# Kernel tuning notes

Measured on AMD Instinct MI355X. Metric: run time of the kernel, lower is better.

Reference implementation:

```python
import jax, jax.numpy as jnp
import numpy as np

N = 100000   # nodes
E = 1600000  # edges (avg degree 16), self-loops added in reference
H = 64       # hidden


def setup_inputs() -> dict:
    key = jax.random.key(0)
    k1, k2, k3, k4, k5 = jax.random.split(key, 5)
    x = jax.random.normal(k1, (N, H), dtype=jnp.float32)
    src = jax.random.randint(k2, (E,), 0, N, dtype=jnp.int32)
    off = jax.random.randint(k3, (E,), 1, N, dtype=jnp.int32)
    dst = (src + off) % N  # guaranteed no self-loops -> matches add_remaining_self_loops
    edge_index = jnp.stack([src, dst])  # row0 = j (source), row1 = i (target)
    # a_i, a_j: Linear(hidden, 1, bias=False) -> weight vectors of shape [H]
    w_i = jax.random.normal(k4, (H,), dtype=jnp.float32) / np.sqrt(H)
    w_j = jax.random.normal(k5, (H,), dtype=jnp.float32) / np.sqrt(H)
    return {"x": x, "edge_index": edge_index, "w_i": w_i, "w_j": w_j}


def reference(x, edge_index, w_i, w_j):
    n = x.shape[0]
    # add_remaining_self_loops: append (v, v) for every node (inputs have none)
    loops = jnp.arange(n, dtype=edge_index.dtype)
    src = jnp.concatenate([edge_index[0], loops])  # j
    dst = jnp.concatenate([edge_index[1], loops])  # i
    # per-node attention scalars, then per-edge gather
    s_i = x @ w_i  # [N]
    s_j = x @ w_j  # [N]
    e = jax.nn.leaky_relu(s_i[dst] + s_j[src], 0.01)  # [E+N]
    # segment softmax over destination node i (every segment non-empty via self-loop)
    e_max = jax.ops.segment_max(e, dst, num_segments=n)
    e_exp = jnp.exp(e - e_max[dst])
    denom = jax.ops.segment_sum(e_exp, dst, num_segments=n)
    alpha = e_exp / denom[dst]  # [E+N]
    # spmm: out[i] = sum_j alpha_ij * x[j], then ReLU
    out = jax.ops.segment_sum(alpha[:, None] * x[src], dst, num_segments=n)
    return jax.nn.relu(out)
```

## Files before the change

kernel.cpp:

```cpp
#include <hip/hip_runtime.h>

#define H 64
#define H4 16
#define H8 8
#define NBUCK 391
#define CAP 4608
#define BIN_BLOCKS 196
#define NODE_PER_BLK 16

typedef _Float16 half8 __attribute__((ext_vector_type(8)));


__global__ __launch_bounds__(1024) void gat_nodebin_kernel(
        const float* __restrict__ x,
        const float* __restrict__ w_i, const float* __restrict__ w_j,
        float* __restrict__ s_i, float* __restrict__ s_j,
        _Float16* __restrict__ xh,
        const int4* __restrict__ src4, const int4* __restrict__ dst4,
        int* __restrict__ cursor, int* __restrict__ buckets,
        int e4, int n) {
    __shared__ int hist[NBUCK];
    __shared__ int boff[NBUCK];
    __shared__ int boff0[NBUCK];
    __shared__ int gbase[NBUCK];
    __shared__ int wtot[16];
    __shared__ int stage[8192];

    int tid = threadIdx.x;
    int lane = tid & 63, wv = tid >> 6;

    if (blockIdx.x >= BIN_BLOCKS) {
        int node = (blockIdx.x - BIN_BLOCKS) * NODE_PER_BLK + wv;
        if (node >= n) return;
        float v = x[(long long)node * H + lane];
        xh[(long long)node * H + lane] = (_Float16)v;
        float a = v * w_i[lane];
        float b = v * w_j[lane];
        #pragma unroll
        for (int off = 32; off > 0; off >>= 1) {
            a += __shfl_down(a, off, 64);
            b += __shfl_down(b, off, 64);
        }
        if (lane == 0) { s_i[node] = a; s_j[node] = b; }
        return;
    }

    if (tid < NBUCK) hist[tid] = 0;
    __syncthreads();

    int4 s[2], d[2];
    bool val[2];
    #pragma unroll
    for (int r = 0; r < 2; ++r) {
        int i4 = blockIdx.x * 2048 + r * 1024 + tid;
        val[r] = (i4 < e4);
        if (val[r]) { s[r] = src4[i4]; d[r] = dst4[i4]; }
        else        { s[r] = make_int4(0,0,0,0); d[r] = make_int4(0,0,0,0); }
    }
    #pragma unroll
    for (int r = 0; r < 2; ++r) if (val[r]) {
        atomicAdd(&hist[d[r].x >> 8], 1);
        atomicAdd(&hist[d[r].y >> 8], 1);
        atomicAdd(&hist[d[r].z >> 8], 1);
        atomicAdd(&hist[d[r].w >> 8], 1);
    }
    __syncthreads();

    if (tid < NBUCK) gbase[tid] = atomicAdd(&cursor[tid], hist[tid]);

    int v = (tid < NBUCK) ? hist[tid] : 0;
    int incl = v;
    #pragma unroll
    for (int off = 1; off < 64; off <<= 1) {
        int t = __shfl_up(incl, off, 64);
        if (lane >= off) incl += t;
    }
    if (lane == 63) wtot[wv] = incl;
    __syncthreads();
    if (tid < NBUCK) {
        int wpref = 0;
        #pragma unroll
        for (int j = 0; j < 16; ++j) wpref += (j < wv) ? wtot[j] : 0;
        int excl = wpref + incl - v;
        boff[tid]  = excl;
        boff0[tid] = excl;
    }
    __syncthreads();

    #pragma unroll
    for (int r = 0; r < 2; ++r) if (val[r]) {
        int ss[4] = {s[r].x, s[r].y, s[r].z, s[r].w};
        int dd[4] = {d[r].x, d[r].y, d[r].z, d[r].w};
        #pragma unroll
        for (int c = 0; c < 4; ++c) {
            int b = dd[c] >> 8;
            int pos = atomicAdd(&boff[b], 1);
            stage[pos] = ((dd[c] & 255) << 17) | ss[c];
        }
    }
    __syncthreads();

    for (int b = wv; b < NBUCK; b += 16) {
        int sbase = boff0[b];
        int L = boff[b] - sbase;
        int gb = gbase[b];
        int* dstp = buckets + (long long)b * CAP + gb;
        for (int i = lane; i < L; i += 64)
            dstp[i] = stage[sbase + i];
    }
}

__global__ __launch_bounds__(1024) void gat_sort_kernel(
        const int* __restrict__ cursor, int* __restrict__ buckets,
        int* __restrict__ row_start, int* __restrict__ count, int n) {
    __shared__ int hist[256];
    __shared__ int offs[256];
    __shared__ int stage[CAP];
    __shared__ int stage2[CAP];
    __shared__ int wtot[4];

    int b = blockIdx.x;
    int tid = threadIdx.x;
    int cnt = cursor[b];
    int* bk = buckets + (long long)b * CAP;

    if (tid < 256) hist[tid] = 0;
    __syncthreads();

    for (int i = tid; i < cnt; i += 1024) {
        int w = bk[i];
        stage[i] = w;
        atomicAdd(&hist[(w >> 17) & 255], 1);
    }
    __syncthreads();

    int lane = tid & 63, wv = tid >> 6;
    int v = (tid < 256) ? hist[tid] : 0;
    int incl = v;
    #pragma unroll
    for (int off = 1; off < 64; off <<= 1) {
        int t = __shfl_up(incl, off, 64);
        if (lane >= off) incl += t;
    }
    if (tid < 256 && lane == 63) wtot[wv] = incl;
    __syncthreads();
    if (tid < 256) {
        int wpref = 0;
        #pragma unroll
        for (int j = 0; j < 4; ++j) wpref += (j < wv) ? wtot[j] : 0;
        int excl = wpref + incl - v;
        offs[tid] = excl;
        int node = (b << 8) + tid;
        if (node < n) {
            row_start[node] = b * CAP + excl;
            count[node] = v;
        }
    }
    __syncthreads();

    for (int i = tid; i < cnt; i += 1024) {
        int w = stage[i];
        int pos = atomicAdd(&offs[(w >> 17) & 255], 1);
        stage2[pos] = w & 0x1FFFF;
    }
    __syncthreads();

    for (int i = tid; i < cnt; i += 1024)
        bk[i] = stage2[i];
}

__global__ __launch_bounds__(256) void gat_aggregate_kernel(
        const float4* __restrict__ x4,
        const half8* __restrict__ xh8,
        const float* __restrict__ s_i,
        const float* __restrict__ s_j,
        const int* __restrict__ row_start,
        const int* __restrict__ count,
        const int* __restrict__ csr_src,
        float4* __restrict__ out4, int n) {
    int wid = (blockIdx.x * blockDim.x + threadIdx.x) >> 6;
    int lane = threadIdx.x & 63;
    int sub = lane >> 4;
    int l16 = lane & 15;
    int g2 = l16 >> 3;
    int q = lane & 7;

    int node = wid * 4 + sub;
    bool vnode = (node < n);
    int nsafe = vnode ? node : 0;
    float sii = s_i[nsafe];
    int start = vnode ? row_start[nsafe] : 0;
    int cnt = vnode ? count[nsafe] : 0;

    float acc[8];
    #pragma unroll
    for (int i = 0; i < 8; ++i) acc[i] = 0.f;
    float den = 0.f;

    for (int base = 0; base < cnt; base += 16) {
        int rem = cnt - base;
        int prsrc = nsafe;
        float wl = 0.f;
        if (l16 < rem) {
            prsrc = csr_src[start + base + l16];
            float e = sii + s_j[prsrc];
            e = (e >= 0.f) ? e : 0.01f * e;
            wl = __expf(e);
        }
        int sb[8]; float wb[8]; half8 hv[8];
        #pragma unroll
        for (int j = 0; j < 8; ++j) {
            int k = (sub << 4) + g2 + 2 * j;
            sb[j] = __shfl(prsrc, k, 64);
            wb[j] = __shfl(wl, k, 64);
        }
        #pragma unroll
        for (int j = 0; j < 8; ++j)
            hv[j] = xh8[(long long)sb[j] * H8 + q];
        #pragma unroll
        for (int j = 0; j < 8; ++j) {
            #pragma unroll
            for (int i = 0; i < 8; ++i)
                acc[i] = fmaf(wb[j], (float)hv[j][i], acc[i]);
            den += wb[j];
        }
    }

    #pragma unroll
    for (int i = 0; i < 8; ++i) acc[i] += __shfl_xor(acc[i], 8, 64);
    den += __shfl_xor(den, 8, 64);

    if (vnode && g2 == 0) {
        float sjn = s_j[node];
        float e0 = sii + sjn; e0 = (e0 >= 0.f) ? e0 : 0.01f * e0;
        float w0 = __expf(e0);
        float4 xa = x4[(long long)node * H4 + 2 * q];
        float4 xb = x4[(long long)node * H4 + 2 * q + 1];
        float dinv = 1.f / (den + w0);
        float4 oa, ob;
        oa.x = (acc[0] + w0 * xa.x) * dinv;
        oa.y = (acc[1] + w0 * xa.y) * dinv;
        oa.z = (acc[2] + w0 * xa.z) * dinv;
        oa.w = (acc[3] + w0 * xa.w) * dinv;
        ob.x = (acc[4] + w0 * xb.x) * dinv;
        ob.y = (acc[5] + w0 * xb.y) * dinv;
        ob.z = (acc[6] + w0 * xb.z) * dinv;
        ob.w = (acc[7] + w0 * xb.w) * dinv;
        oa.x = (oa.x > 0.f) ? oa.x : 0.f;
        oa.y = (oa.y > 0.f) ? oa.y : 0.f;
        oa.z = (oa.z > 0.f) ? oa.z : 0.f;
        oa.w = (oa.w > 0.f) ? oa.w : 0.f;
        ob.x = (ob.x > 0.f) ? ob.x : 0.f;
        ob.y = (ob.y > 0.f) ? ob.y : 0.f;
        ob.z = (ob.z > 0.f) ? ob.z : 0.f;
        ob.w = (ob.w > 0.f) ? ob.w : 0.f;
        out4[(long long)node * H4 + 2 * q]     = oa;
        out4[(long long)node * H4 + 2 * q + 1] = ob;
    }
}

extern "C" void kernel_launch(void* const* d_in, const int* in_sizes, int n_in,
                              void* d_out, int out_size, void* d_ws, size_t ws_size,
                              hipStream_t stream) {
    const float* x    = (const float*)d_in[0];
    const int*   edge = (const int*)  d_in[1];
    const float* w_i  = (const float*)d_in[2];
    const float* w_j  = (const float*)d_in[3];

    int n     = in_sizes[0] / H;
    int e_cnt = in_sizes[1] / 2;
    const int* src = edge;
    const int* dst = edge + e_cnt;

    float* out = (float*)d_out;

    char* ws = (char*)d_ws;
    float*    s_i       = (float*)ws;     ws += (size_t)n * 4;
    float*    s_j       = (float*)ws;     ws += (size_t)n * 4;
    int*      cursor    = (int*)ws;       ws += 512 * 4;
    int*      row_start = (int*)ws;       ws += (size_t)n * 4;
    int*      count     = (int*)ws;       ws += (size_t)n * 4;
    int*      buckets   = (int*)ws;       ws += (size_t)NBUCK * CAP * 4;
    _Float16* xh        = (_Float16*)ws;

    int e4 = e_cnt / 4;
    int node_blocks = (n + NODE_PER_BLK - 1) / NODE_PER_BLK;
    int fused_blocks = BIN_BLOCKS + node_blocks;

    hipMemsetAsync(cursor, 0, 512 * 4, stream);

    gat_nodebin_kernel<<<fused_blocks, 1024, 0, stream>>>(
        x, w_i, w_j, s_i, s_j, xh,
        (const int4*)src, (const int4*)dst, cursor, buckets, e4, n);

    gat_sort_kernel<<<NBUCK, 1024, 0, stream>>>(
        cursor, buckets, row_start, count, n);

    int waves = (n + 3) / 4;
    long long agg_threads = (long long)waves * 64;
    gat_aggregate_kernel<<<(unsigned)((agg_threads + 255) / 256), 256, 0, stream>>>(
        (const float4*)x, (const half8*)xh, s_i, s_j, row_start, count, buckets,
        (float4*)out, n);
}
```

Baseline: 151.6 us.

## Fuse per-bucket sort with aggregation, keeping sorted edges and weights in LDS

The separate sort kernel and aggregate kernel are merged into one kernel with one block per bucket of 256 destination nodes. The block counting-sorts the bucket's edges into shared memory and precomputes each edge's exp weight there, then aggregates its nodes directly from LDS. This removes a kernel launch, the global write and re-read of the sorted CSR, and the row_start/count arrays. In exchange, only 391 blocks of 512 threads are launched, so each block walks 256 nodes in sequence, and occupancy may be limited by the 36KB of LDS per block.

```diff
diff --git a/kernel.cpp b/kernel.cpp
--- a/kernel.cpp
+++ b/kernel.cpp
@@ -110,152 +110,164 @@
     }
 }
 
-__global__ __launch_bounds__(1024) void gat_sort_kernel(
-        const int* __restrict__ cursor, int* __restrict__ buckets,
-        int* __restrict__ row_start, int* __restrict__ count, int n) {
-    __shared__ int hist[256];
-    __shared__ int offs[256];
-    __shared__ int stage[CAP];
-    __shared__ int stage2[CAP];
-    __shared__ int wtot[4];
-
-    int b = blockIdx.x;
-    int tid = threadIdx.x;
-    int cnt = cursor[b];
-    int* bk = buckets + (long long)b * CAP;
-
-    if (tid < 256) hist[tid] = 0;
-    __syncthreads();
-
-    for (int i = tid; i < cnt; i += 1024) {
-        int w = bk[i];
-        stage[i] = w;
-        atomicAdd(&hist[(w >> 17) & 255], 1);
-    }
-    __syncthreads();
-
-    int lane = tid & 63, wv = tid >> 6;
-    int v = (tid < 256) ? hist[tid] : 0;
-    int incl = v;
-    #pragma unroll
-    for (int off = 1; off < 64; off <<= 1) {
-        int t = __shfl_up(incl, off, 64);
-        if (lane >= off) incl += t;
-    }
-    if (tid < 256 && lane == 63) wtot[wv] = incl;
-    __syncthreads();
-    if (tid < 256) {
-        int wpref = 0;
-        #pragma unroll
-        for (int j = 0; j < 4; ++j) wpref += (j < wv) ? wtot[j] : 0;
-        int excl = wpref + incl - v;
-        offs[tid] = excl;
-        int node = (b << 8) + tid;
-        if (node < n) {
-            row_start[node] = b * CAP + excl;
-            count[node] = v;
-        }
-    }
-    __syncthreads();
-
-    for (int i = tid; i < cnt; i += 1024) {
-        int w = stage[i];
-        int pos = atomicAdd(&offs[(w >> 17) & 255], 1);
-        stage2[pos] = w & 0x1FFFF;
-    }
-    __syncthreads();
-
-    for (int i = tid; i < cnt; i += 1024)
-        bk[i] = stage2[i];
-}
-
-__global__ __launch_bounds__(256) void gat_aggregate_kernel(
+__global__ __launch_bounds__(512, 4) void gat_sortagg_kernel(
         const float4* __restrict__ x4,
         const half8* __restrict__ xh8,
         const float* __restrict__ s_i,
         const float* __restrict__ s_j,
-        const int* __restrict__ row_start,
-        const int* __restrict__ count,
-        const int* __restrict__ csr_src,
+        const int* __restrict__ cursor,
+        const int* __restrict__ buckets,
         float4* __restrict__ out4, int n) {
-    int wid = (blockIdx.x * blockDim.x + threadIdx.x) >> 6;
-    int lane = threadIdx.x & 63;
+    __shared__ int   hist[256];
+    __shared__ int   offs[256];
+    __shared__ int   start0[256];
+    __shared__ float sii[256];
+    __shared__ int   wtot[8];
+    __shared__ int2  ew[CAP];
+
+    int b = blockIdx.x;
+    int tid = threadIdx.x;
+    int lane = tid & 63, wv = tid >> 6;
+    int cnt_b = cursor[b];
+    if (cnt_b > CAP) cnt_b = CAP;
+    const int* bk = buckets + (long long)b * CAP;
+
+    if (tid < 256) {
+        hist[tid] = 0;
+        int node = (b << 8) + tid;
+        sii[tid] = (node < n) ? s_i[node] : 0.f;
+    }
+    __syncthreads();
+
+    for (int i = tid; i < cnt_b; i += 512)
+        atomicAdd(&hist[(bk[i] >> 17) & 255], 1);
+    __syncthreads();
+
+    int v = (tid < 256) ? hist[tid] : 0;
+    int incl = v;
+    #pragma unroll
+    for (int off = 1; off < 64; off <<= 1) {
+        int t = __shfl_up(incl, off, 64);
+        if (lane >= off) incl += t;
+    }
+    if (tid < 256 && lane == 63) wtot[wv] = incl;
+    __syncthreads();
+    if (tid < 256) {
+        int wpref = 0;
+        #pragma unroll
+        for (int j = 0; j < 4; ++j) wpref += (j < wv) ? wtot[j] : 0;
+        int excl = wpref + incl - v;
+        offs[tid]   = excl;
+        start0[tid] = excl;
+    }
+    __syncthreads();
+
+    for (int i = tid; i < cnt_b; i += 512) {
+        int w = bk[i];
+        int loc = (w >> 17) & 255;
+        int src = w & 0x1FFFF;
+        float e = sii[loc] + s_j[src];
+        e = (e >= 0.f) ? e : 0.01f * e;
+        float we = __expf(e);
+        int pos = atomicAdd(&offs[loc], 1);
+        ew[pos] = make_int2(src, __float_as_int(we));
+    }
+    __syncthreads();
+
     int sub = lane >> 4;
-    int l16 = lane & 15;
-    int g2 = l16 >> 3;
-    int q = lane & 7;
-
-    int node = wid * 4 + sub;
-    bool vnode = (node < n);
-    int nsafe = vnode ? node : 0;
-    float sii = s_i[nsafe];
-    int start = vnode ? row_start[nsafe] : 0;
-    int cnt = vnode ? count[nsafe] : 0;
-
-    float acc[8];
-    #pragma unroll
-    for (int i = 0; i < 8; ++i) acc[i] = 0.f;
-    float den = 0.f;
-
-    for (int base = 0; base < cnt; base += 16) {
-        int rem = cnt - base;
-        int prsrc = nsafe;
-        float wl = 0.f;
-        if (l16 < rem) {
-            prsrc = csr_src[start + base + l16];
-            float e = sii + s_j[prsrc];
-            e = (e >= 0.f) ? e : 0.01f * e;
-            wl = __expf(e);
+    int g2  = (lane >> 3) & 1;
+    int q   = lane & 7;
+
+    for (int rr = 0; rr < 8; ++rr) {
+        int loc  = rr * 32 + wv * 4 + sub;
+        int node = (b << 8) + loc;
+        bool vnode = (node < n);
+        int ls   = start0[loc];
+        int cntn = vnode ? hist[loc] : 0;
+
+        float acc[8];
+        #pragma unroll
+        for (int i = 0; i < 8; ++i) acc[i] = 0.f;
+        float den = 0.f;
+
+        for (int base = 0; base < cntn; base += 16) {
+            int rem = cntn - base;
+            int lsb = ls + base + g2;
+            if (rem >= 16) {
+                int sb[8]; float wb[8]; half8 hv[8];
+                #pragma unroll
+                for (int j = 0; j < 8; ++j) {
+                    int2 e = ew[lsb + 2 * j];
+                    sb[j] = e.x; wb[j] = __int_as_float(e.y);
+                }
+                #pragma unroll
+                for (int j = 0; j < 8; ++j)
+                    hv[j] = xh8[(long long)sb[j] * H8 + q];
+                #pragma unroll
+                for (int j = 0; j < 8; ++j) {
+                    #pragma unroll
+                    for (int i = 0; i < 8; ++i)
+                        acc[i] = fmaf(wb[j], (float)hv[j][i], acc[i]);
+                    den += wb[j];
+                }
+            } else {
+                int sb[8]; float wb[8]; half8 hv[8];
+                #pragma unroll
+                for (int j = 0; j < 8; ++j) {
+                    int slot = g2 + 2 * j;
+                    sb[j] = -1; wb[j] = 0.f;
+                    if (slot < rem) {
+                        int2 e = ew[lsb + 2 * j];
+                        sb[j] = e.x; wb[j] = __int_as_float(e.y);
+                    }
+                }
+                #pragma unroll
+                for (int j = 0; j < 8; ++j)
+                    if (sb[j] >= 0)
+                        hv[j] = xh8[(long long)sb[j] * H8 + q];
+                #pragma unroll
+                for (int j = 0; j < 8; ++j) {
+                    if (sb[j] >= 0) {
+                        #pragma unroll
+                        for (int i = 0; i < 8; ++i)
+                            acc[i] = fmaf(wb[j], (float)hv[j][i], acc[i]);
+                        den += wb[j];
+                    }
+                }
+            }
         }
-        int sb[8]; float wb[8]; half8 hv[8];
-        #pragma unroll
-        for (int j = 0; j < 8; ++j) {
-            int k = (sub << 4) + g2 + 2 * j;
-            sb[j] = __shfl(prsrc, k, 64);
-            wb[j] = __shfl(wl, k, 64);
+
+        #pragma unroll
+        for (int i = 0; i < 8; ++i) acc[i] += __shfl_xor(acc[i], 8, 64);
+        den += __shfl_xor(den, 8, 64);
+
+        if (vnode && g2 == 0) {
+            float sjn = s_j[node];
+            float e0 = sii[loc] + sjn; e0 = (e0 >= 0.f) ? e0 : 0.01f * e0;
+            float w0 = __expf(e0);
+            float4 xa = x4[(long long)node * H4 + 2 * q];
+            float4 xb = x4[(long long)node * H4 + 2 * q + 1];
+            float dinv = 1.f / (den + w0);
+            float4 oa, ob;
+            oa.x = (acc[0] + w0 * xa.x) * dinv;
+            oa.y = (acc[1] + w0 * xa.y) * dinv;
+            oa.z = (acc[2] + w0 * xa.z) * dinv;
+            oa.w = (acc[3] + w0 * xa.w) * dinv;
+            ob.x = (acc[4] + w0 * xb.x) * dinv;
+            ob.y = (acc[5] + w0 * xb.y) * dinv;
+            ob.z = (acc[6] + w0 * xb.z) * dinv;
+            ob.w = (acc[7] + w0 * xb.w) * dinv;
+            oa.x = (oa.x > 0.f) ? oa.x : 0.f;
+            oa.y = (oa.y > 0.f) ? oa.y : 0.f;
+            oa.z = (oa.z > 0.f) ? oa.z : 0.f;
+            oa.w = (oa.w > 0.f) ? oa.w : 0.f;
+            ob.x = (ob.x > 0.f) ? ob.x : 0.f;
+            ob.y = (ob.y > 0.f) ? ob.y : 0.f;
+            ob.z = (ob.z > 0.f) ? ob.z : 0.f;
+            ob.w = (ob.w > 0.f) ? ob.w : 0.f;
+            out4[(long long)node * H4 + 2 * q]     = oa;
+            out4[(long long)node * H4 + 2 * q + 1] = ob;
         }
-        #pragma unroll
-        for (int j = 0; j < 8; ++j)
-            hv[j] = xh8[(long long)sb[j] * H8 + q];
-        #pragma unroll
-        for (int j = 0; j < 8; ++j) {
-            #pragma unroll
-            for (int i = 0; i < 8; ++i)
-                acc[i] = fmaf(wb[j], (float)hv[j][i], acc[i]);
-            den += wb[j];
-        }
-    }
-
-    #pragma unroll
-    for (int i = 0; i < 8; ++i) acc[i] += __shfl_xor(acc[i], 8, 64);
-    den += __shfl_xor(den, 8, 64);
-
-    if (vnode && g2 == 0) {
-        float sjn = s_j[node];
-        float e0 = sii + sjn; e0 = (e0 >= 0.f) ? e0 : 0.01f * e0;
-        float w0 = __expf(e0);
-        float4 xa = x4[(long long)node * H4 + 2 * q];
-        float4 xb = x4[(long long)node * H4 + 2 * q + 1];
-        float dinv = 1.f / (den + w0);
-        float4 oa, ob;
-        oa.x = (acc[0] + w0 * xa.x) * dinv;
-        oa.y = (acc[1] + w0 * xa.y) * dinv;
-        oa.z = (acc[2] + w0 * xa.z) * dinv;
-        oa.w = (acc[3] + w0 * xa.w) * dinv;
-        ob.x = (acc[4] + w0 * xb.x) * dinv;
-        ob.y = (acc[5] + w0 * xb.y) * dinv;
-        ob.z = (acc[6] + w0 * xb.z) * dinv;
-        ob.w = (acc[7] + w0 * xb.w) * dinv;
-        oa.x = (oa.x > 0.f) ? oa.x : 0.f;
-        oa.y = (oa.y > 0.f) ? oa.y : 0.f;
-        oa.z = (oa.z > 0.f) ? oa.z : 0.f;
-        oa.w = (oa.w > 0.f) ? oa.w : 0.f;
-        ob.x = (ob.x > 0.f) ? ob.x : 0.f;
-        ob.y = (ob.y > 0.f) ? ob.y : 0.f;
-        ob.z = (ob.z > 0.f) ? ob.z : 0.f;
-        ob.w = (ob.w > 0.f) ? ob.w : 0.f;
-        out4[(long long)node * H4 + 2 * q]     = oa;
-        out4[(long long)node * H4 + 2 * q + 1] = ob;
     }
 }
 
@@ -278,8 +290,6 @@
     float*    s_i       = (float*)ws;     ws += (size_t)n * 4;
     float*    s_j       = (float*)ws;     ws += (size_t)n * 4;
     int*      cursor    = (int*)ws;       ws += 512 * 4;
-    int*      row_start = (int*)ws;       ws += (size_t)n * 4;
-    int*      count     = (int*)ws;       ws += (size_t)n * 4;
     int*      buckets   = (int*)ws;       ws += (size_t)NBUCK * CAP * 4;
     _Float16* xh        = (_Float16*)ws;
 
@@ -293,12 +303,7 @@
         x, w_i, w_j, s_i, s_j, xh,
         (const int4*)src, (const int4*)dst, cursor, buckets, e4, n);
 
-    gat_sort_kernel<<<NBUCK, 1024, 0, stream>>>(
-        cursor, buckets, row_start, count, n);
-
-    int waves = (n + 3) / 4;
-    long long agg_threads = (long long)waves * 64;
-    gat_aggregate_kernel<<<(unsigned)((agg_threads + 255) / 256), 256, 0, stream>>>(
-        (const float4*)x, (const half8*)xh, s_i, s_j, row_start, count, buckets,
+    gat_sortagg_kernel<<<NBUCK, 512, 0, stream>>>(
+        (const float4*)x, (const half8*)xh, s_i, s_j, cursor, buckets,
         (float4*)out, n);
 }
```

New measurement: 151.5 us. Within noise of the previous version (-0.1%).
